# Optimization experiments

Hardware: AMD Instinct MI355X
Metric: run time of the kernel (lower is better)

The kernel has to match this reference:

```python
import jax, jax.numpy as jnp
import numpy as np


def _conv_same(x, k):
    # x: [C, H, W] single sample; k: [C_out, C_in, 3, 3] per-sample kernel
    return jax.lax.conv_general_dilated(
        x[None], k, window_strides=(1, 1), padding='SAME',
        dimension_numbers=('NCHW', 'OIHW', 'NCHW'))[0]


_batched_conv = jax.vmap(_conv_same)  # maps over batch of inputs and batch of kernels


def setup_inputs() -> dict:
    key = jax.random.key(0)
    k1, k2, k3 = jax.random.split(key, 3)
    B, C, H, W = 16, 256, 64, 64
    x = jax.random.normal(k1, (B, C, H, W), dtype=jnp.float32)
    # scale kernels down so pre-relu activations stay in a sane range
    kernel1 = jax.random.normal(k2, (B, C, C, 3, 3), dtype=jnp.float32) * 0.02
    kernel2 = jax.random.normal(k3, (B, C, C, 3, 3), dtype=jnp.float32) * 0.02
    return {"x": x, "kernel1": kernel1, "kernel2": kernel2}


def reference(x, kernel1, kernel2):
    # per-sample conv1 -> relu -> per-sample conv2 -> residual add -> relu
    h = jax.nn.relu(_batched_conv(x, kernel1))          # [B, C, H, W]
    out = jax.nn.relu(x + _batched_conv(h, kernel2))    # [B, C, H, W]
    return out
```

## Files before the change

### kernel.cpp

```cpp
#include <hip/hip_runtime.h>
#include <hip/hip_bf16.h>
#include <stdint.h>

typedef __attribute__((ext_vector_type(8))) short bf16x8;
typedef __attribute__((ext_vector_type(4))) float f32x4;
typedef __attribute__((address_space(1))) const void g_void;
typedef __attribute__((address_space(3))) void l_void;

#define NB 16
#define NC 256
#define NHW 4096
#define NT 72
#define SLOTB 32768

__global__ __launch_bounds__(256) void prep_xt2(const float* __restrict__ x,
                                                __hip_bfloat16* __restrict__ xt2,
                                                float* __restrict__ zp) {
  __shared__ float tile[64][65];
  const int b = blockIdx.z;
  const int cb = blockIdx.y << 6;
  const int pb = blockIdx.x << 6;
  if (blockIdx.x == 0 && blockIdx.y == 0 && blockIdx.z == 0) {
#pragma unroll
    for (int q = 0; q < 8; ++q) zp[(q << 8) + threadIdx.x] = 0.f;
  }
  const float* xs = x + ((size_t)(b * NC + cb) << 12) + pb;
#pragma unroll
  for (int k = 0; k < 16; ++k) {
    int idx = threadIdx.x + (k << 8);
    int c = idx >> 6, p = idx & 63;
    tile[p][c] = xs[((size_t)c << 12) + p];
  }
  __syncthreads();
#pragma unroll
  for (int k = 0; k < 16; ++k) {
    int idx = threadIdx.x + (k << 8);
    int p = idx >> 6, c = idx & 63;
    int P = pb + p, C = cb + c;
    xt2[((size_t)(b * 8 + (C >> 5)) << 17) + ((size_t)P << 5) + (C & 31)] =
        __float2bfloat16(tile[p][c]);
  }
}

__global__ __launch_bounds__(256) void prep_kt2(const float* __restrict__ kin,
                                                __hip_bfloat16* __restrict__ kt2) {
  const int bco = blockIdx.x;
  const int b = bco >> 8, co = bco & 255;
  const size_t base = (size_t)bco * 2304;
  const int ci = threadIdx.x;
  float v[9];
#pragma unroll
  for (int s = 0; s < 9; ++s) v[s] = kin[base + ci * 9 + s];
  const int cib = ci >> 5, chunk = (ci >> 3) & 3, e = ci & 7;
  const int sc = chunk ^ ((co >> 1) & 3);
#pragma unroll
  for (int s = 0; s < 9; ++s) {
    const size_t dst = (((size_t)(b * NT + cib * 9 + s)) << 13) +
                       (co << 5) + (sc << 3) + e;
    kt2[dst] = __float2bfloat16(v[s]);
  }
}

template <int PASS>
__global__ __launch_bounds__(512, 2) void conv_gemm(
    const __hip_bfloat16* __restrict__ img2,
    const __hip_bfloat16* __restrict__ kt2,
    const float* __restrict__ xres,
    const __hip_bfloat16* __restrict__ zp,
    void* __restrict__ outp) {
  __shared__ __align__(16) char L[3 * SLOTB];

  const int tid = threadIdx.x;
  const int lane = tid & 63;
  const int wid = tid >> 6;
  const int wm = wid >> 2;
  const int wn = wid & 3;

  const int orig = blockIdx.x;
  const int g = ((orig & 7) << 5) + (orig >> 3);
  const int b = g >> 4;
  const int ptile = g & 15;
  const int pbase = ptile << 8;

  const char* xb = (const char*)img2 + ((size_t)b << 21);
  const char* ktb = (const char*)kt2 + ((size_t)(b * NT) << 14);
  const char* zpb = (const char*)zp;

  const int srow = lane >> 2;
  const int sch = (lane & 3) ^ ((srow >> 1) & 3);

  int aoff[8], boff[4];
#pragma unroll
  for (int i = 0; i < 8; ++i) {
    const int ma = (wm << 7) + (i << 4) + (lane & 15);
    aoff[i] = (ma << 6) + ((((lane >> 4) ^ ((ma >> 1) & 3))) << 4);
  }
#pragma unroll
  for (int j = 0; j < 4; ++j) {
    const int nb = (wn << 6) + (j << 4) + (lane & 15);
    boff[j] = (nb << 6) + ((((lane >> 4) ^ ((nb >> 1) & 3))) << 4);
  }
  const bool killlo = (lane & 15) == 0;
  const bool killhi = (lane & 15) == 15;
  const bf16x8 z8 = {0, 0, 0, 0, 0, 0, 0, 0};

  f32x4 acc[8][4];
#pragma unroll
  for (int i = 0; i < 8; ++i)
#pragma unroll
    for (int j = 0; j < 4; ++j) acc[i][j] = (f32x4){0.f, 0.f, 0.f, 0.f};

  auto stageI = [&](int tn, int cibp, int dh, int dw, bool dummy) {
    char* dst0 = L + (tn % 3) * SLOTB;
    const char* cb = xb + ((size_t)(cibp & 7) << 18);
#pragma unroll
    for (int i = 0; i < 2; ++i) {
      const int grp = (i << 3) + wid;
      const int h = (ptile << 2) + (grp >> 2) + dh;
      const bool ok = !dummy && ((unsigned)h < 64u);
      const int off = ((pbase + (grp << 4) + srow + (dh << 6) + dw) << 6) + (sch << 4);
      const char* src = ok ? cb + off : zpb + (lane << 4);
      __builtin_amdgcn_global_load_lds((g_void*)src, (l_void*)(dst0 + (grp << 10)), 16, 0, 0);
    }
  };
  auto stageKer = [&](int tn, bool dummy) {
    char* dst0 = L + (tn % 3) * SLOTB + 16384;
    const char* src0 = ktb + ((size_t)tn << 14);
#pragma unroll
    for (int i = 0; i < 2; ++i) {
      const int grp = (i << 3) + wid;
      const char* src = !dummy ? src0 + (grp << 10) + (lane << 4) : zpb + (lane << 4);
      __builtin_amdgcn_global_load_lds((g_void*)src, (l_void*)(dst0 + (grp << 10)), 16, 0, 0);
    }
  };
  auto stageBoth = [&](int tn, int cibp, int dh, int dw, bool dummy) {
    stageI(tn, cibp, dh, dw, dummy);
    stageKer(tn, dummy);
  };

  stageBoth(0, 0, -1, -1, false);
  stageBoth(1, 0, -1, 0, false);
  asm volatile("s_waitcnt vmcnt(4)" ::: "memory");
  __builtin_amdgcn_s_barrier();
  __builtin_amdgcn_sched_barrier(0);

#pragma unroll 1
  for (int c9 = 0; c9 < 8; ++c9) {
#pragma unroll
    for (int s = 0; s < 9; ++s) {
      const int kk = c9 * 9 + s;
      const int sl = s % 3;
      const char* At = L + sl * SLOTB + ((PASS == 1) ? 0 : 16384);
      const char* Bt = L + sl * SLOTB + ((PASS == 1) ? 16384 : 0);
      const int dw = s % 3 - 1;

      bf16x8 fa[8], fb[4];
#pragma unroll
      for (int i = 0; i < 8; ++i) fa[i] = *(const bf16x8*)(At + aoff[i]);
#pragma unroll
      for (int j = 0; j < 4; ++j) fb[j] = *(const bf16x8*)(Bt + boff[j]);
      {
        const int s2 = (s + 2) % 9;
        stageBoth(kk + 2, c9 + (s + 2) / 9, s2 / 3 - 1, s2 % 3 - 1, kk + 2 >= NT);
      }
      __builtin_amdgcn_s_barrier();
      asm volatile("s_waitcnt lgkmcnt(0)" ::: "memory");
      __builtin_amdgcn_sched_barrier(0);
      if (PASS == 1) {
        if (dw == -1) {
          fa[0] = killlo ? z8 : fa[0];
          fa[4] = killlo ? z8 : fa[4];
        }
        if (dw == 1) {
          fa[3] = killhi ? z8 : fa[3];
          fa[7] = killhi ? z8 : fa[7];
        }
      } else {
        if (dw == -1) fb[0] = killlo ? z8 : fb[0];
        if (dw == 1) fb[3] = killhi ? z8 : fb[3];
      }
      __builtin_amdgcn_s_setprio(1);
#pragma unroll
      for (int i = 0; i < 8; ++i)
#pragma unroll
        for (int j = 0; j < 4; ++j)
          acc[i][j] = __builtin_amdgcn_mfma_f32_16x16x32_bf16(fa[i], fb[j], acc[i][j], 0, 0, 0);
      __builtin_amdgcn_s_setprio(0);
      asm volatile("s_waitcnt vmcnt(4)" ::: "memory");
      __builtin_amdgcn_s_barrier();
      __builtin_amdgcn_sched_barrier(0);
    }
  }
  asm volatile("s_waitcnt vmcnt(0)" ::: "memory");
  __builtin_amdgcn_sched_barrier(0);

  const int lg = lane >> 4;
  const int ln = lane & 15;
  if (PASS == 1) {
    __hip_bfloat16* ho = (__hip_bfloat16*)outp;
#pragma unroll
    for (int i = 0; i < 8; ++i)
#pragma unroll
      for (int j = 0; j < 4; ++j)
#pragma unroll
        for (int r = 0; r < 4; ++r) {
          int pixel = pbase + (wm << 7) + (i << 4) + (lg << 2) + r;
          int co = (wn << 6) + (j << 4) + ln;
          float v = acc[i][j][r];
          v = v > 0.f ? v : 0.f;
          ho[((size_t)(b * 8 + (co >> 5)) << 17) + ((size_t)pixel << 5) + (co & 31)] =
              __float2bfloat16(v);
        }
  } else {
    float* oo = (float*)outp;
#pragma unroll
    for (int i = 0; i < 8; ++i)
#pragma unroll
      for (int j = 0; j < 4; ++j)
#pragma unroll
        for (int r = 0; r < 4; ++r) {
          int co = (wm << 7) + (i << 4) + (lg << 2) + r;
          int pixel = pbase + (wn << 6) + (j << 4) + ln;
          size_t idx = ((size_t)(b * NC + co) << 12) + pixel;
          float v = acc[i][j][r] + xres[idx];
          oo[idx] = v > 0.f ? v : 0.f;
        }
  }
}

extern "C" void kernel_launch(void* const* d_in, const int* in_sizes, int n_in,
                              void* d_out, int out_size, void* d_ws, size_t ws_size,
                              hipStream_t stream) {
  const float* x = (const float*)d_in[0];
  const float* k1 = (const float*)d_in[1];
  const float* k2 = (const float*)d_in[2];

  char* w = (char*)d_ws;
  __hip_bfloat16* xt2 = (__hip_bfloat16*)(w + 256);
  __hip_bfloat16* ht2 = xt2 + (size_t)NB * 8 * NHW * 32;
  __hip_bfloat16* kt2 = ht2 + (size_t)NB * 8 * NHW * 32;
  float* zp = (float*)(kt2 + (size_t)NB * NT * 256 * 32);

  prep_xt2<<<dim3(64, 4, NB), 256, 0, stream>>>(x, xt2, zp);
  prep_kt2<<<dim3(NB * NC), 256, 0, stream>>>(k1, kt2);
  conv_gemm<1><<<dim3(256), 512, 0, stream>>>(xt2, kt2, nullptr,
                                              (const __hip_bfloat16*)zp, (void*)ht2);
  prep_kt2<<<dim3(NB * NC), 256, 0, stream>>>(k2, kt2);
  conv_gemm<2><<<dim3(256), 512, 0, stream>>>(ht2, kt2, x,
                                              (const __hip_bfloat16*)zp, d_out);
}
```

Measured before the change: 183.4 us.

## Interleave LDS fragment reads with MFMA groups and drop a barrier per step

The K-loop is restructured so that each step has a single barrier, placed at its start after the vmcnt wait, instead of two. The twelve LDS fragment reads are issued up front. MFMA groups then start as partial lgkmcnt waits confirm their A fragments have arrived. Global-to-LDS staging for step kk+2 is moved in after the first two MFMA rows, so it overlaps compute. This aims to hide LDS read latency and cut barrier stalls, but it depends on precise hand-placed waitcnt and sched_barrier ordering, and any slip there would read stale fragments.

```diff
diff --git a/kernel.cpp b/kernel.cpp
--- a/kernel.cpp
+++ b/kernel.cpp
@@ -140,9 +140,6 @@
 
   stageBoth(0, 0, -1, -1, false);
   stageBoth(1, 0, -1, 0, false);
-  asm volatile("s_waitcnt vmcnt(4)" ::: "memory");
-  __builtin_amdgcn_s_barrier();
-  __builtin_amdgcn_sched_barrier(0);
 
 #pragma unroll 1
   for (int c9 = 0; c9 < 8; ++c9) {
@@ -154,40 +151,83 @@
       const char* Bt = L + sl * SLOTB + ((PASS == 1) ? 16384 : 0);
       const int dw = s % 3 - 1;
 
-      bf16x8 fa[8], fb[4];
-#pragma unroll
-      for (int i = 0; i < 8; ++i) fa[i] = *(const bf16x8*)(At + aoff[i]);
-#pragma unroll
-      for (int j = 0; j < 4; ++j) fb[j] = *(const bf16x8*)(Bt + boff[j]);
-      {
-        const int s2 = (s + 2) % 9;
-        stageBoth(kk + 2, c9 + (s + 2) / 9, s2 / 3 - 1, s2 % 3 - 1, kk + 2 >= NT);
-      }
+      asm volatile("s_waitcnt vmcnt(4)" ::: "memory");
       __builtin_amdgcn_s_barrier();
-      asm volatile("s_waitcnt lgkmcnt(0)" ::: "memory");
+      __builtin_amdgcn_sched_barrier(0);
+
+      bf16x8 fb[4], fa[8];
+      fb[0] = *(const bf16x8*)(Bt + boff[0]);
+      fb[1] = *(const bf16x8*)(Bt + boff[1]);
+      fb[2] = *(const bf16x8*)(Bt + boff[2]);
+      fb[3] = *(const bf16x8*)(Bt + boff[3]);
+      fa[0] = *(const bf16x8*)(At + aoff[0]);
+      fa[1] = *(const bf16x8*)(At + aoff[1]);
+      __builtin_amdgcn_sched_barrier(0);
+      fa[2] = *(const bf16x8*)(At + aoff[2]);
+      fa[3] = *(const bf16x8*)(At + aoff[3]);
+      __builtin_amdgcn_sched_barrier(0);
+      fa[4] = *(const bf16x8*)(At + aoff[4]);
+      fa[5] = *(const bf16x8*)(At + aoff[5]);
+      __builtin_amdgcn_sched_barrier(0);
+      fa[6] = *(const bf16x8*)(At + aoff[6]);
+      fa[7] = *(const bf16x8*)(At + aoff[7]);
+      __builtin_amdgcn_sched_barrier(0);
+
+      asm volatile("s_waitcnt lgkmcnt(6)" ::: "memory");
       __builtin_amdgcn_sched_barrier(0);
       if (PASS == 1) {
-        if (dw == -1) {
-          fa[0] = killlo ? z8 : fa[0];
-          fa[4] = killlo ? z8 : fa[4];
-        }
-        if (dw == 1) {
-          fa[3] = killhi ? z8 : fa[3];
-          fa[7] = killhi ? z8 : fa[7];
-        }
+        if (dw == -1) fa[0] = killlo ? z8 : fa[0];
       } else {
         if (dw == -1) fb[0] = killlo ? z8 : fb[0];
         if (dw == 1) fb[3] = killhi ? z8 : fb[3];
       }
       __builtin_amdgcn_s_setprio(1);
 #pragma unroll
-      for (int i = 0; i < 8; ++i)
-#pragma unroll
-        for (int j = 0; j < 4; ++j)
-          acc[i][j] = __builtin_amdgcn_mfma_f32_16x16x32_bf16(fa[i], fb[j], acc[i][j], 0, 0, 0);
+      for (int j = 0; j < 4; ++j)
+        acc[0][j] = __builtin_amdgcn_mfma_f32_16x16x32_bf16(fa[0], fb[j], acc[0][j], 0, 0, 0);
+#pragma unroll
+      for (int j = 0; j < 4; ++j)
+        acc[1][j] = __builtin_amdgcn_mfma_f32_16x16x32_bf16(fa[1], fb[j], acc[1][j], 0, 0, 0);
+      __builtin_amdgcn_sched_barrier(0);
+
+      {
+        const int s2 = (s + 2) % 9;
+        stageBoth(kk + 2, c9 + (s + 2) / 9, s2 / 3 - 1, s2 % 3 - 1, kk + 2 >= NT);
+      }
+      __builtin_amdgcn_sched_barrier(0);
+
+      asm volatile("s_waitcnt lgkmcnt(4)" ::: "memory");
+      __builtin_amdgcn_sched_barrier(0);
+      if (PASS == 1 && dw == 1) fa[3] = killhi ? z8 : fa[3];
+#pragma unroll
+      for (int j = 0; j < 4; ++j)
+        acc[2][j] = __builtin_amdgcn_mfma_f32_16x16x32_bf16(fa[2], fb[j], acc[2][j], 0, 0, 0);
+#pragma unroll
+      for (int j = 0; j < 4; ++j)
+        acc[3][j] = __builtin_amdgcn_mfma_f32_16x16x32_bf16(fa[3], fb[j], acc[3][j], 0, 0, 0);
+      __builtin_amdgcn_sched_barrier(0);
+
+      asm volatile("s_waitcnt lgkmcnt(2)" ::: "memory");
+      __builtin_amdgcn_sched_barrier(0);
+      if (PASS == 1 && dw == -1) fa[4] = killlo ? z8 : fa[4];
+#pragma unroll
+      for (int j = 0; j < 4; ++j)
+        acc[4][j] = __builtin_amdgcn_mfma_f32_16x16x32_bf16(fa[4], fb[j], acc[4][j], 0, 0, 0);
+#pragma unroll
+      for (int j = 0; j < 4; ++j)
+        acc[5][j] = __builtin_amdgcn_mfma_f32_16x16x32_bf16(fa[5], fb[j], acc[5][j], 0, 0, 0);
+      __builtin_amdgcn_sched_barrier(0);
+
+      asm volatile("s_waitcnt lgkmcnt(0)" ::: "memory");
+      __builtin_amdgcn_sched_barrier(0);
+      if (PASS == 1 && dw == 1) fa[7] = killhi ? z8 : fa[7];
+#pragma unroll
+      for (int j = 0; j < 4; ++j)
+        acc[6][j] = __builtin_amdgcn_mfma_f32_16x16x32_bf16(fa[6], fb[j], acc[6][j], 0, 0, 0);
+#pragma unroll
+      for (int j = 0; j < 4; ++j)
+        acc[7][j] = __builtin_amdgcn_mfma_f32_16x16x32_bf16(fa[7], fb[j], acc[7][j], 0, 0, 0);
       __builtin_amdgcn_s_setprio(0);
-      asm volatile("s_waitcnt vmcnt(4)" ::: "memory");
-      __builtin_amdgcn_s_barrier();
       __builtin_amdgcn_sched_barrier(0);
     }
   }
```

Result: faster. 175.4 us (-4.4%).
